# Kernel tuning notes

Measured on AMD Instinct MI355X. Metric: run time of the kernel, lower is better.

## Reference

```python
import jax, jax.numpy as jnp
import numpy as np

B, S, D, H = 4, 1024, 1024, 16
HD = D // H  # head_dim = 64
MASKED_BIAS = -10000.0


def setup_inputs() -> dict:
    key = jax.random.key(0)
    ks = jax.random.split(key, 7)
    sc = 0.02
    return {
        "hidden_states": jax.random.normal(ks[0], (B, S, D), jnp.float32),
        "textual_key": jax.random.normal(ks[1], (B, H, S, HD), jnp.float32),
        "textual_value": jax.random.normal(ks[2], (B, H, S, HD), jnp.float32),
        "Wc": jax.random.normal(ks[3], (D, 3 * D), jnp.float32) * sc,  # Conv1D c_attn
        "bc": jnp.zeros((3 * D,), jnp.float32),
        "Wp": jax.random.normal(ks[4], (D, D), jnp.float32) * sc,  # Conv1D c_proj
        "bp": jnp.zeros((D,), jnp.float32),
    }


def reference(hidden_states, textual_key, textual_value, Wc, bc, Wp, bp):
    b, s, d = hidden_states.shape
    # Conv1D: x @ W + b, then split into q, k, v
    qkv = hidden_states @ Wc + bc  # [B,S,3D]
    q, k, v = jnp.split(qkv, 3, axis=-1)

    def split_heads(t):  # [B,S,D] -> [B,H,S,HD]
        return t.reshape(b, s, H, HD).transpose(0, 2, 1, 3)

    q, k, v = split_heads(q), split_heads(k), split_heads(v)

    # cross-key scores against textual past + fused elementwise self-term
    text_w = jnp.einsum("bhqd,bhkd->bhqk", q, textual_key)  # [B,H,S,S_kv]
    self_w = jnp.sum(q * k, axis=-1, keepdims=True)  # [B,H,S,1]
    attn_w = jnp.concatenate([text_w, self_w], axis=-1) / (HD ** 0.5)

    # nonResidual causal mask: bias[kl-ql:kl, 1:kl+1] (strict lower-tri since
    # columns are shifted by 1) concatenated with an always-true self column
    i = jnp.arange(s)
    causal = i[None, :] < i[:, None]  # [S,S_kv]: allow k < q (strict)
    mask = jnp.concatenate([causal, jnp.ones((s, 1), bool)], axis=-1)[None, None]
    attn_w = jnp.where(mask, attn_w, jnp.asarray(MASKED_BIAS, attn_w.dtype))
    attn_w = jax.nn.softmax(attn_w, axis=-1)

    w_rest, w_self = attn_w[..., :-1], attn_w[..., -1:]
    out = jnp.einsum("bhqk,bhkd->bhqd", w_rest, textual_value) + w_self * v

    out = out.transpose(0, 2, 1, 3).reshape(b, s, d)  # merge heads
    return out @ Wp + bp
```

## Files before the change

kernel.cpp:

```cpp
#include <hip/hip_runtime.h>

typedef __bf16 bf16_t;
typedef __bf16 bf16x8 __attribute__((ext_vector_type(8)));
typedef __bf16 bf16x4 __attribute__((ext_vector_type(4)));
typedef _Float16 f16x4 __attribute__((ext_vector_type(4)));
typedef _Float16 f16x8 __attribute__((ext_vector_type(8)));
typedef float f32x4 __attribute__((ext_vector_type(4)));

__device__ __forceinline__ void gl_lds16(const void* g, void* l) {
  __builtin_amdgcn_global_load_lds(
      (const __attribute__((address_space(1))) unsigned int*)g,
      (__attribute__((address_space(3))) unsigned int*)l, 16, 0, 0);
}

__global__ __launch_bounds__(256) void prep_kernel(
    const float* __restrict__ hs, const float* __restrict__ tk, const float* __restrict__ tv,
    const float* __restrict__ Wc, const float* __restrict__ Wp,
    bf16_t* __restrict__ Ahs, bf16_t* __restrict__ Ktb, _Float16* __restrict__ Vtb,
    bf16_t* __restrict__ WcT, bf16_t* __restrict__ WpT) {
  const int blk = blockIdx.x;
  const int tid = threadIdx.x;
  if (blk < 4096) {
    const float4* src = (blk < 2048) ? (const float4*)hs : (const float4*)tk;
    bf16x8* dst = (blk < 2048) ? (bf16x8*)Ahs : (bf16x8*)Ktb;
    int i = (blk & 2047) * 256 + tid;
    float4 v0 = src[2 * i], v1 = src[2 * i + 1];
    bf16x8 o;
    o[0] = (bf16_t)v0.x; o[1] = (bf16_t)v0.y; o[2] = (bf16_t)v0.z; o[3] = (bf16_t)v0.w;
    o[4] = (bf16_t)v1.x; o[5] = (bf16_t)v1.y; o[6] = (bf16_t)v1.z; o[7] = (bf16_t)v1.w;
    dst[i] = o;
  } else {
    __shared__ float tile[32][65];
    const float* in; bf16_t* out; int C, r0, c0; size_t base = 0; bool isV = false;
    if (blk < 5632) {
      int t = blk - 4096; in = Wc; out = WcT; C = 3072;
      r0 = (t / 96) * 64; c0 = (t % 96) * 32;
    } else if (blk < 6144) {
      int t = blk - 5632; in = Wp; out = WpT; C = 1024;
      r0 = (t >> 5) * 64; c0 = (t & 31) * 32;
    } else {
      int t = blk - 6144; int z = t >> 5, rest = t & 31;
      in = tv; out = nullptr; isV = true; C = 64; base = (size_t)z * 65536;
      r0 = (rest >> 1) * 64; c0 = (rest & 1) * 32;
    }
    {
      int rr = tid >> 2, cq = (tid & 3) << 3;
      const float* sp = in + base + (size_t)(r0 + rr) * C + c0 + cq;
      float4 v0 = *(const float4*)sp, v1 = *(const float4*)(sp + 4);
      tile[cq + 0][rr] = v0.x; tile[cq + 1][rr] = v0.y;
      tile[cq + 2][rr] = v0.z; tile[cq + 3][rr] = v0.w;
      tile[cq + 4][rr] = v1.x; tile[cq + 5][rr] = v1.y;
      tile[cq + 6][rr] = v1.z; tile[cq + 7][rr] = v1.w;
    }
    __syncthreads();
    int y = tid >> 3, l = tid & 7;
    if (isV) {
      f16x8 o;
#pragma unroll
      for (int j = 0; j < 8; j++) {
        int k = ((l & 4) << 3) | ((j & 4) << 2) | ((l & 2) << 2) | ((l & 1) << 2) | (j & 3);
        o[j] = (_Float16)tile[y][k];
      }
      *(f16x8*)(Vtb + base + (size_t)(c0 + y) * 1024 + r0 + (l << 3)) = o;
    } else {
      const float* rowp = &tile[y][l << 3];
      bf16x8 o;
#pragma unroll
      for (int j = 0; j < 8; j++) o[j] = (bf16_t)rowp[j];
      *(bf16x8*)(out + (size_t)(c0 + y) * 1024 + r0 + (l << 3)) = o;
    }
  }
}

#define ATTN_M 12.0f
__global__ __launch_bounds__(512, 4) void fused_attn_kernel(
    const bf16_t* __restrict__ Ahs, const bf16_t* __restrict__ WcT,
    const float* __restrict__ bc,
    const bf16_t* __restrict__ Ktxt, const _Float16* __restrict__ VtxtT,
    bf16_t* __restrict__ Aout) {
  const int bh = blockIdx.x;
  const int y = blockIdx.y;
  const int qt = (y < 4) ? y : 11 - y;
  const int b = bh >> 4, h = bh & 15;
  const int tid = threadIdx.x, wave = tid >> 6, lane = tid & 63;
  const int c = lane & 15, qd = lane >> 4;
  const int i_base = qt * 128 + wave * 16;
  const int kt_max = 2 * qt + 1;
  const int m0 = b * 1024 + qt * 128;

  const bf16_t* Ktb = Ktxt + (size_t)bh * 65536;
  const _Float16* Vtb = VtxtT + (size_t)bh * 65536;

  __shared__ __align__(16) char pool[49152];
  bf16_t* Asm = (bf16_t*)pool;
  bf16_t* Bsm = (bf16_t*)(pool + 16384);
  bf16_t* Qsm = (bf16_t*)pool;
  bf16_t* KsmB = (bf16_t*)(pool + 16384);
  _Float16* VsmB = (_Float16*)(pool + 32768);

  f32x4 acc[12];
#pragma unroll
  for (int j = 0; j < 12; j++) acc[j] = (f32x4){0.f, 0.f, 0.f, 0.f};

  for (int kt = 0; kt < 16; kt++) {
#pragma unroll
    for (int p = 0; p < 2; p++) {
      int chunk = p * 512 + tid;
      int row = chunk >> 3, sb = chunk & 7, kb = sb ^ (row & 7);
      gl_lds16(Ahs + (size_t)(m0 + row) * 1024 + kt * 64 + kb * 8, Asm + chunk * 8);
    }
#pragma unroll
    for (int p = 0; p < 3; p++) {
      int chunk = p * 512 + tid;
      int brow = chunk >> 3, sb = chunk & 7, kb = sb ^ (brow & 7);
      int wrow = (brow >> 6) * 1024 + h * 64 + (brow & 63);
      gl_lds16(WcT + (size_t)wrow * 1024 + kt * 64 + kb * 8, Bsm + chunk * 8);
    }
    __syncthreads();
#pragma unroll
    for (int kk = 0; kk < 2; kk++) {
      int arow = wave * 16 + c;
      bf16x8 af = *(const bf16x8*)(&Asm[arow * 64 + (((4 * kk + qd) ^ (arow & 7)) << 3)]);
#pragma unroll
      for (int j = 0; j < 12; j++) {
        int brow = 16 * j + c;
        bf16x8 bf = *(const bf16x8*)(&Bsm[brow * 64 + (((4 * kk + qd) ^ (brow & 7)) << 3)]);
        acc[j] = __builtin_amdgcn_mfma_f32_16x16x32_bf16(af, bf, acc[j], 0, 0, 0);
      }
    }
    __syncthreads();
  }

  {
    int row = tid >> 3, sb = tid & 7, kb = sb ^ (row & 7);
    gl_lds16(Ktb + (size_t)row * 64 + kb * 8, KsmB + tid * 8);
    gl_lds16(Vtb + (size_t)row * 1024 + kb * 8, VsmB + tid * 8);
  }

#pragma unroll
  for (int j = 0; j < 12; j++) {
    float bv = bc[(j >> 2) * 1024 + h * 64 + 16 * (j & 3) + c];
#pragma unroll
    for (int r = 0; r < 4; r++) acc[j][r] += bv;
  }

  float wself[4];
#pragma unroll
  for (int r = 0; r < 4; r++) {
    float part = acc[0][r] * acc[4][r] + acc[1][r] * acc[5][r] +
                 acc[2][r] * acc[6][r] + acc[3][r] * acc[7][r];
#pragma unroll
    for (int mk = 1; mk < 16; mk <<= 1) part += __shfl_xor(part, mk, 64);
    wself[r] = __expf(part * 0.125f - ATTN_M);
  }

  f32x4 O[4];
#pragma unroll
  for (int u = 0; u < 4; u++)
#pragma unroll
    for (int r = 0; r < 4; r++) O[u][r] = wself[r] * acc[8 + u][r];

  bf16_t* Qw = Qsm + wave * 1024;
#pragma unroll
  for (int j = 0; j < 4; j++) {
#pragma unroll
    for (int r = 0; r < 4; r++) {
      int ql = 4 * qd + r, d = 16 * j + c;
      int ch = (d >> 3) ^ (ql & 7);
      Qw[ql * 64 + (ch << 3) + (d & 7)] = (bf16_t)acc[j][r];
    }
  }
  bf16x8 aq[2];
#pragma unroll
  for (int kk = 0; kk < 2; kk++) {
    int ch = (4 * kk + qd) ^ (c & 7);
    aq[kk] = *(const bf16x8*)(&Qw[c * 64 + (ch << 3)]);
  }

  float l_loc = 0.f;
  for (int kt = 0; kt <= kt_max; kt++) {
    __syncthreads();
    if (kt < kt_max) {
      int nb = (kt + 1) & 1;
      int row = tid >> 3, sb = tid & 7, kb = sb ^ (row & 7);
      gl_lds16(Ktb + (size_t)((kt + 1) * 64 + row) * 64 + kb * 8, KsmB + nb * 4096 + tid * 8);
      gl_lds16(Vtb + (size_t)row * 1024 + (kt + 1) * 64 + kb * 8, VsmB + nb * 4096 + tid * 8);
    }
    if (64 * kt >= i_base + 16) continue;
    const bf16_t* Ks = KsmB + (kt & 1) * 4096;
    const _Float16* Vs = VsmB + (kt & 1) * 4096;

    f32x4 sc[4];
#pragma unroll
    for (int t = 0; t < 4; t++) sc[t] = (f32x4){0.f, 0.f, 0.f, 0.f};
#pragma unroll
    for (int kk = 0; kk < 2; kk++) {
#pragma unroll
      for (int t = 0; t < 4; t++) {
        int row = 16 * t + c;
        bf16x8 bk = *(const bf16x8*)(&Ks[row * 64 + (((4 * kk + qd) ^ (row & 7)) << 3)]);
        sc[t] = __builtin_amdgcn_mfma_f32_16x16x32_bf16(bk, aq[kk], sc[t], 0, 0, 0);
      }
    }
    const bool edge = (64 * kt + 63 >= i_base);
    f16x4 pa[4];
    if (!edge) {
#pragma unroll
      for (int t = 0; t < 4; t++)
#pragma unroll
        for (int r = 0; r < 4; r++) {
          float p = __expf(sc[t][r] * 0.125f - ATTN_M);
          l_loc += p;
          pa[t][r] = (_Float16)p;
        }
    } else {
#pragma unroll
      for (int t = 0; t < 4; t++)
#pragma unroll
        for (int r = 0; r < 4; r++) {
          bool masked = (64 * kt + 16 * t + 4 * qd + r >= i_base + c);
          float p = masked ? 0.f : __expf(sc[t][r] * 0.125f - ATTN_M);
          l_loc += p;
          pa[t][r] = (_Float16)p;
        }
    }
#pragma unroll
    for (int tp = 0; tp < 2; tp++) {
#pragma unroll
      for (int u = 0; u < 4; u++) {
        int row = 16 * u + c;
        f16x8 vv = *(const f16x8*)(&Vs[row * 64 + (((4 * tp + qd) ^ (row & 7)) << 3)]);
        f16x4 vlo = __builtin_shufflevector(vv, vv, 0, 1, 2, 3);
        f16x4 vhi = __builtin_shufflevector(vv, vv, 4, 5, 6, 7);
        O[u] = __builtin_amdgcn_mfma_f32_16x16x16f16(pa[2 * tp], vlo, O[u], 0, 0, 0);
        O[u] = __builtin_amdgcn_mfma_f32_16x16x16f16(pa[2 * tp + 1], vhi, O[u], 0, 0, 0);
      }
    }
  }

  l_loc += __shfl_xor(l_loc, 16, 64);
  l_loc += __shfl_xor(l_loc, 32, 64);
#pragma unroll
  for (int r = 0; r < 4; r++) {
    float lq = __shfl(l_loc, 4 * qd + r, 16);
    float inv = 1.0f / (lq + wself[r]);
    int i = i_base + 4 * qd + r;
#pragma unroll
    for (int u = 0; u < 4; u++)
      Aout[((size_t)b * 1024 + i) * 1024 + h * 64 + 16 * u + c] = (bf16_t)(O[u][r] * inv);
  }
}

__global__ __launch_bounds__(256) void gemm_out_kernel(
    const bf16_t* __restrict__ A, const bf16_t* __restrict__ Bt, const float* __restrict__ bias,
    float* __restrict__ out) {
  __shared__ bf16_t Asm[2][4096];
  __shared__ bf16_t Bsm[2][8192];
  const int tid = threadIdx.x;
  const int wave = tid >> 6, lane = tid & 63;
  const int c = lane & 15, qd = lane >> 4;
  const int wn = wave * 32;
  const int m0 = blockIdx.y * 64, n0 = blockIdx.x * 128;

  f32x4 acc[4][2];
#pragma unroll
  for (int i = 0; i < 4; i++)
#pragma unroll
    for (int j = 0; j < 2; j++) acc[i][j] = (f32x4){0.f, 0.f, 0.f, 0.f};

#pragma unroll
  for (int p = 0; p < 2; p++) {
    int chunk = p * 256 + tid;
    int row = chunk >> 3, sb = chunk & 7, kb = sb ^ (row & 7);
    gl_lds16(A + (size_t)(m0 + row) * 1024 + kb * 8, &Asm[0][chunk * 8]);
  }
#pragma unroll
  for (int p = 0; p < 4; p++) {
    int chunk = p * 256 + tid;
    int row = chunk >> 3, sb = chunk & 7, kb = sb ^ (row & 7);
    gl_lds16(Bt + (size_t)(n0 + row) * 1024 + kb * 8, &Bsm[0][chunk * 8]);
  }
  for (int it = 0; it < 16; it++) {
    __syncthreads();
    if (it < 15) {
      int nbuf = (it + 1) & 1, kt = (it + 1) * 64;
#pragma unroll
      for (int p = 0; p < 2; p++) {
        int chunk = p * 256 + tid;
        int row = chunk >> 3, sb = chunk & 7, kb = sb ^ (row & 7);
        gl_lds16(A + (size_t)(m0 + row) * 1024 + kt + kb * 8, &Asm[nbuf][chunk * 8]);
      }
#pragma unroll
      for (int p = 0; p < 4; p++) {
        int chunk = p * 256 + tid;
        int row = chunk >> 3, sb = chunk & 7, kb = sb ^ (row & 7);
        gl_lds16(Bt + (size_t)(n0 + row) * 1024 + kt + kb * 8, &Bsm[nbuf][chunk * 8]);
      }
    }
    const int bs = it & 1;
#pragma unroll
    for (int kk = 0; kk < 2; kk++) {
      bf16x8 af[4], bfr[2];
#pragma unroll
      for (int i = 0; i < 4; i++) {
        int row = 16 * i + c;
        af[i] = *(const bf16x8*)(&Asm[bs][row * 64 + (((4 * kk + qd) ^ (row & 7)) << 3)]);
      }
#pragma unroll
      for (int j = 0; j < 2; j++) {
        int row = wn + 16 * j + c;
        bfr[j] = *(const bf16x8*)(&Bsm[bs][row * 64 + (((4 * kk + qd) ^ (row & 7)) << 3)]);
      }
#pragma unroll
      for (int i = 0; i < 4; i++)
#pragma unroll
        for (int j = 0; j < 2; j++)
          acc[i][j] = __builtin_amdgcn_mfma_f32_16x16x32_bf16(af[i], bfr[j], acc[i][j], 0, 0, 0);
    }
  }
#pragma unroll
  for (int j = 0; j < 2; j++) {
    int n = n0 + wn + 16 * j + c;
    float bv = bias[n];
#pragma unroll
    for (int i = 0; i < 4; i++) {
#pragma unroll
      for (int r = 0; r < 4; r++) {
        int m = m0 + 16 * i + 4 * qd + r;
        out[(size_t)m * 1024 + n] = acc[i][j][r] + bv;
      }
    }
  }
}

extern "C" void kernel_launch(void* const* d_in, const int* in_sizes, int n_in,
                              void* d_out, int out_size, void* d_ws, size_t ws_size,
                              hipStream_t stream) {
  const float* hs = (const float*)d_in[0];
  const float* tk = (const float*)d_in[1];
  const float* tv = (const float*)d_in[2];
  const float* Wc = (const float*)d_in[3];
  const float* bc = (const float*)d_in[4];
  const float* Wp = (const float*)d_in[5];
  const float* bp = (const float*)d_in[6];
  float* out = (float*)d_out;

  bf16_t* ws = (bf16_t*)d_ws;
  const size_t M1 = 1u << 20;
  bf16_t* Ahs  = ws;
  bf16_t* WcT  = ws + 4 * M1;
  bf16_t* WpT  = ws + 7 * M1;
  bf16_t* Ktb  = ws + 8 * M1;
  _Float16* Vtb = (_Float16*)(ws + 12 * M1);
  bf16_t* Aout = ws + 28 * M1;

  prep_kernel<<<8192, 256, 0, stream>>>(hs, tk, tv, Wc, Wp, Ahs, Ktb, Vtb, WcT, WpT);
  fused_attn_kernel<<<dim3(64, 8), 512, 0, stream>>>(Ahs, WcT, bc, Ktb, Vtb, Aout);
  gemm_out_kernel<<<dim3(8, 64), 256, 0, stream>>>(Aout, WpT, bp, out);
}
```

Baseline: 174.7 us.

## Use 2D warp tiling for fused QKV GEMM with 4 waves, 32 queries each

The fused attention kernel drops from 8 waves to 4 waves per block. Each wave now computes a 64x96 sub-tile of the 128x192 QKV projection in a 2D warp layout, instead of a 16x192 strip, so each loaded A/B fragment is reused by more MFMAs and LDS traffic per MFMA falls. The QKV tile is staged through a swizzled LDS buffer so each wave can gather Q, the self-key and V for its 32 query rows. In the attention loop each K/V fragment load now feeds two query groups. The costs are higher register pressure (24 accumulators), an extra LDS round-trip with syncs, and half as many waves per block for latency hiding.

Result: no change. 174.8 us (+0.1%).

```diff
diff --git a/kernel.cpp b/kernel.cpp
--- a/kernel.cpp
+++ b/kernel.cpp
@@ -2,7 +2,6 @@
 
 typedef __bf16 bf16_t;
 typedef __bf16 bf16x8 __attribute__((ext_vector_type(8)));
-typedef __bf16 bf16x4 __attribute__((ext_vector_type(4)));
 typedef _Float16 f16x4 __attribute__((ext_vector_type(4)));
 typedef _Float16 f16x8 __attribute__((ext_vector_type(8)));
 typedef float f32x4 __attribute__((ext_vector_type(4)));
@@ -73,7 +72,7 @@
 }
 
 #define ATTN_M 12.0f
-__global__ __launch_bounds__(512, 4) void fused_attn_kernel(
+__global__ __launch_bounds__(256, 2) void fused_attn_kernel(
     const bf16_t* __restrict__ Ahs, const bf16_t* __restrict__ WcT,
     const float* __restrict__ bc,
     const bf16_t* __restrict__ Ktxt, const _Float16* __restrict__ VtxtT,
@@ -84,9 +83,9 @@
   const int b = bh >> 4, h = bh & 15;
   const int tid = threadIdx.x, wave = tid >> 6, lane = tid & 63;
   const int c = lane & 15, qd = lane >> 4;
-  const int i_base = qt * 128 + wave * 16;
+  const int m0 = b * 1024 + qt * 128;
+  const int i_base2 = qt * 128 + 32 * wave;
   const int kt_max = 2 * qt + 1;
-  const int m0 = b * 1024 + qt * 128;
 
   const bf16_t* Ktb = Ktxt + (size_t)bh * 65536;
   const _Float16* Vtb = VtxtT + (size_t)bh * 65536;
@@ -94,24 +93,27 @@
   __shared__ __align__(16) char pool[49152];
   bf16_t* Asm = (bf16_t*)pool;
   bf16_t* Bsm = (bf16_t*)(pool + 16384);
-  bf16_t* Qsm = (bf16_t*)pool;
-  bf16_t* KsmB = (bf16_t*)(pool + 16384);
-  _Float16* VsmB = (_Float16*)(pool + 32768);
-
-  f32x4 acc[12];
-#pragma unroll
-  for (int j = 0; j < 12; j++) acc[j] = (f32x4){0.f, 0.f, 0.f, 0.f};
+  bf16_t* T = (bf16_t*)pool;
+  bf16_t* KsmB = (bf16_t*)pool;
+  _Float16* VsmB = (_Float16*)(pool + 16384);
+
+  const int wm = (wave & 1) * 64, wn = (wave >> 1) * 96;
+  f32x4 acc[4][6];
+#pragma unroll
+  for (int i = 0; i < 4; i++)
+#pragma unroll
+    for (int j = 0; j < 6; j++) acc[i][j] = (f32x4){0.f, 0.f, 0.f, 0.f};
 
   for (int kt = 0; kt < 16; kt++) {
 #pragma unroll
-    for (int p = 0; p < 2; p++) {
-      int chunk = p * 512 + tid;
+    for (int p = 0; p < 4; p++) {
+      int chunk = p * 256 + tid;
       int row = chunk >> 3, sb = chunk & 7, kb = sb ^ (row & 7);
       gl_lds16(Ahs + (size_t)(m0 + row) * 1024 + kt * 64 + kb * 8, Asm + chunk * 8);
     }
 #pragma unroll
-    for (int p = 0; p < 3; p++) {
-      int chunk = p * 512 + tid;
+    for (int p = 0; p < 6; p++) {
+      int chunk = p * 256 + tid;
       int brow = chunk >> 3, sb = chunk & 7, kb = sb ^ (brow & 7);
       int wrow = (brow >> 6) * 1024 + h * 64 + (brow & 63);
       gl_lds16(WcT + (size_t)wrow * 1024 + kt * 64 + kb * 8, Bsm + chunk * 8);
@@ -119,110 +121,148 @@
     __syncthreads();
 #pragma unroll
     for (int kk = 0; kk < 2; kk++) {
-      int arow = wave * 16 + c;
-      bf16x8 af = *(const bf16x8*)(&Asm[arow * 64 + (((4 * kk + qd) ^ (arow & 7)) << 3)]);
-#pragma unroll
-      for (int j = 0; j < 12; j++) {
-        int brow = 16 * j + c;
-        bf16x8 bf = *(const bf16x8*)(&Bsm[brow * 64 + (((4 * kk + qd) ^ (brow & 7)) << 3)]);
-        acc[j] = __builtin_amdgcn_mfma_f32_16x16x32_bf16(af, bf, acc[j], 0, 0, 0);
-      }
+      bf16x8 af[4], bfr[6];
+#pragma unroll
+      for (int i = 0; i < 4; i++) {
+        int row = wm + 16 * i + c;
+        af[i] = *(const bf16x8*)(&Asm[row * 64 + (((4 * kk + qd) ^ (row & 7)) << 3)]);
+      }
+#pragma unroll
+      for (int j = 0; j < 6; j++) {
+        int row = wn + 16 * j + c;
+        bfr[j] = *(const bf16x8*)(&Bsm[row * 64 + (((4 * kk + qd) ^ (row & 7)) << 3)]);
+      }
+#pragma unroll
+      for (int i = 0; i < 4; i++)
+#pragma unroll
+        for (int j = 0; j < 6; j++)
+          acc[i][j] = __builtin_amdgcn_mfma_f32_16x16x32_bf16(af[i], bfr[j], acc[i][j], 0, 0, 0);
     }
     __syncthreads();
   }
 
-  {
-    int row = tid >> 3, sb = tid & 7, kb = sb ^ (row & 7);
-    gl_lds16(Ktb + (size_t)row * 64 + kb * 8, KsmB + tid * 8);
-    gl_lds16(Vtb + (size_t)row * 1024 + kb * 8, VsmB + tid * 8);
-  }
-
-#pragma unroll
-  for (int j = 0; j < 12; j++) {
-    float bv = bc[(j >> 2) * 1024 + h * 64 + 16 * (j & 3) + c];
-#pragma unroll
-    for (int r = 0; r < 4; r++) acc[j][r] += bv;
-  }
-
-  float wself[4];
-#pragma unroll
-  for (int r = 0; r < 4; r++) {
-    float part = acc[0][r] * acc[4][r] + acc[1][r] * acc[5][r] +
-                 acc[2][r] * acc[6][r] + acc[3][r] * acc[7][r];
-#pragma unroll
-    for (int mk = 1; mk < 16; mk <<= 1) part += __shfl_xor(part, mk, 64);
-    wself[r] = __expf(part * 0.125f - ATTN_M);
-  }
-
-  f32x4 O[4];
-#pragma unroll
-  for (int u = 0; u < 4; u++)
-#pragma unroll
-    for (int r = 0; r < 4; r++) O[u][r] = wself[r] * acc[8 + u][r];
-
-  bf16_t* Qw = Qsm + wave * 1024;
-#pragma unroll
-  for (int j = 0; j < 4; j++) {
-#pragma unroll
-    for (int r = 0; r < 4; r++) {
-      int ql = 4 * qd + r, d = 16 * j + c;
-      int ch = (d >> 3) ^ (ql & 7);
-      Qw[ql * 64 + (ch << 3) + (d & 7)] = (bf16_t)acc[j][r];
-    }
-  }
-  bf16x8 aq[2];
-#pragma unroll
-  for (int kk = 0; kk < 2; kk++) {
-    int ch = (4 * kk + qd) ^ (c & 7);
-    aq[kk] = *(const bf16x8*)(&Qw[c * 64 + (ch << 3)]);
-  }
-
-  float l_loc = 0.f;
+#pragma unroll
+  for (int j = 0; j < 6; j++) {
+    int col = wn + 16 * j + c;
+    float bv = bc[(col >> 6) * 1024 + h * 64 + (col & 63)];
+    int chq = (col >> 3) & 24;
+    int chl = (col >> 3) & 7;
+#pragma unroll
+    for (int i = 0; i < 4; i++) {
+#pragma unroll
+      for (int r = 0; r < 4; r++) {
+        int row = wm + 16 * i + 4 * qd + r;
+        int ch = chq | (chl ^ (row & 7));
+        T[row * 192 + ch * 8 + (col & 7)] = (bf16_t)(acc[i][j][r] + bv);
+      }
+    }
+  }
+  __syncthreads();
+
+  bf16x8 aq[2][2];
+  float wsc[2];
+  float ws[2][4];
+#pragma unroll
+  for (int g = 0; g < 2; g++) {
+    int row = 32 * wave + 16 * g + c;
+    float part = 0.f;
+#pragma unroll
+    for (int kk = 0; kk < 2; kk++) {
+      int ch = (4 * kk + qd) ^ (row & 7);
+      aq[g][kk] = *(const bf16x8*)(&T[row * 192 + ch * 8]);
+      bf16x8 kf = *(const bf16x8*)(&T[row * 192 + (8 | ch) * 8]);
+#pragma unroll
+      for (int jj = 0; jj < 8; jj++) part += (float)aq[g][kk][jj] * (float)kf[jj];
+    }
+    part += __shfl_xor(part, 16, 64);
+    part += __shfl_xor(part, 32, 64);
+    wsc[g] = __expf(part * 0.125f - ATTN_M);
+#pragma unroll
+    for (int r = 0; r < 4; r++) ws[g][r] = __shfl(wsc[g], 4 * qd + r, 16);
+  }
+  f32x4 O[2][4];
+#pragma unroll
+  for (int g = 0; g < 2; g++) {
+#pragma unroll
+    for (int u = 0; u < 4; u++) {
+#pragma unroll
+      for (int r = 0; r < 4; r++) {
+        int row = 32 * wave + 16 * g + 4 * qd + r;
+        int ch = 16 | ((2 * u + (c >> 3)) ^ (row & 7));
+        O[g][u][r] = ws[g][r] * (float)T[row * 192 + ch * 8 + (c & 7)];
+      }
+    }
+  }
+  __syncthreads();
+
+#pragma unroll
+  for (int p = 0; p < 2; p++) {
+    int chunk = p * 256 + tid;
+    int row = chunk >> 3, sb = chunk & 7, kb = sb ^ (row & 7);
+    gl_lds16(Ktb + (size_t)row * 64 + kb * 8, KsmB + chunk * 8);
+    gl_lds16(Vtb + (size_t)row * 1024 + kb * 8, VsmB + chunk * 8);
+  }
+
+  float l_loc[2] = {0.f, 0.f};
   for (int kt = 0; kt <= kt_max; kt++) {
     __syncthreads();
     if (kt < kt_max) {
       int nb = (kt + 1) & 1;
-      int row = tid >> 3, sb = tid & 7, kb = sb ^ (row & 7);
-      gl_lds16(Ktb + (size_t)((kt + 1) * 64 + row) * 64 + kb * 8, KsmB + nb * 4096 + tid * 8);
-      gl_lds16(Vtb + (size_t)row * 1024 + (kt + 1) * 64 + kb * 8, VsmB + nb * 4096 + tid * 8);
-    }
-    if (64 * kt >= i_base + 16) continue;
+#pragma unroll
+      for (int p = 0; p < 2; p++) {
+        int chunk = p * 256 + tid;
+        int row = chunk >> 3, sb = chunk & 7, kb = sb ^ (row & 7);
+        gl_lds16(Ktb + (size_t)((kt + 1) * 64 + row) * 64 + kb * 8,
+                 KsmB + nb * 4096 + chunk * 8);
+        gl_lds16(Vtb + (size_t)row * 1024 + (kt + 1) * 64 + kb * 8,
+                 VsmB + nb * 4096 + chunk * 8);
+      }
+    }
+    if (64 * kt >= i_base2 + 32) continue;
     const bf16_t* Ks = KsmB + (kt & 1) * 4096;
     const _Float16* Vs = VsmB + (kt & 1) * 4096;
 
-    f32x4 sc[4];
-#pragma unroll
-    for (int t = 0; t < 4; t++) sc[t] = (f32x4){0.f, 0.f, 0.f, 0.f};
+    f32x4 sc[2][4];
+#pragma unroll
+    for (int t = 0; t < 4; t++) {
+      sc[0][t] = (f32x4){0.f, 0.f, 0.f, 0.f};
+      sc[1][t] = (f32x4){0.f, 0.f, 0.f, 0.f};
+    }
 #pragma unroll
     for (int kk = 0; kk < 2; kk++) {
 #pragma unroll
       for (int t = 0; t < 4; t++) {
         int row = 16 * t + c;
         bf16x8 bk = *(const bf16x8*)(&Ks[row * 64 + (((4 * kk + qd) ^ (row & 7)) << 3)]);
-        sc[t] = __builtin_amdgcn_mfma_f32_16x16x32_bf16(bk, aq[kk], sc[t], 0, 0, 0);
-      }
-    }
-    const bool edge = (64 * kt + 63 >= i_base);
-    f16x4 pa[4];
+        sc[0][t] = __builtin_amdgcn_mfma_f32_16x16x32_bf16(bk, aq[0][kk], sc[0][t], 0, 0, 0);
+        sc[1][t] = __builtin_amdgcn_mfma_f32_16x16x32_bf16(bk, aq[1][kk], sc[1][t], 0, 0, 0);
+      }
+    }
+    const bool edge = (64 * kt + 63 >= i_base2);
+    f16x4 pa[2][4];
     if (!edge) {
 #pragma unroll
-      for (int t = 0; t < 4; t++)
-#pragma unroll
-        for (int r = 0; r < 4; r++) {
-          float p = __expf(sc[t][r] * 0.125f - ATTN_M);
-          l_loc += p;
-          pa[t][r] = (_Float16)p;
-        }
+      for (int g = 0; g < 2; g++)
+#pragma unroll
+        for (int t = 0; t < 4; t++)
+#pragma unroll
+          for (int r = 0; r < 4; r++) {
+            float p = __expf(sc[g][t][r] * 0.125f - ATTN_M);
+            l_loc[g] += p;
+            pa[g][t][r] = (_Float16)p;
+          }
     } else {
 #pragma unroll
-      for (int t = 0; t < 4; t++)
-#pragma unroll
-        for (int r = 0; r < 4; r++) {
-          bool masked = (64 * kt + 16 * t + 4 * qd + r >= i_base + c);
-          float p = masked ? 0.f : __expf(sc[t][r] * 0.125f - ATTN_M);
-          l_loc += p;
-          pa[t][r] = (_Float16)p;
-        }
+      for (int g = 0; g < 2; g++)
+#pragma unroll
+        for (int t = 0; t < 4; t++)
+#pragma unroll
+          for (int r = 0; r < 4; r++) {
+            bool masked = (64 * kt + 16 * t + 4 * qd + r >= i_base2 + 16 * g + c);
+            float p = masked ? 0.f : __expf(sc[g][t][r] * 0.125f - ATTN_M);
+            l_loc[g] += p;
+            pa[g][t][r] = (_Float16)p;
+          }
     }
 #pragma unroll
     for (int tp = 0; tp < 2; tp++) {
@@ -232,22 +272,28 @@
         f16x8 vv = *(const f16x8*)(&Vs[row * 64 + (((4 * tp + qd) ^ (row & 7)) << 3)]);
         f16x4 vlo = __builtin_shufflevector(vv, vv, 0, 1, 2, 3);
         f16x4 vhi = __builtin_shufflevector(vv, vv, 4, 5, 6, 7);
-        O[u] = __builtin_amdgcn_mfma_f32_16x16x16f16(pa[2 * tp], vlo, O[u], 0, 0, 0);
-        O[u] = __builtin_amdgcn_mfma_f32_16x16x16f16(pa[2 * tp + 1], vhi, O[u], 0, 0, 0);
-      }
-    }
-  }
-
-  l_loc += __shfl_xor(l_loc, 16, 64);
-  l_loc += __shfl_xor(l_loc, 32, 64);
-#pragma unroll
-  for (int r = 0; r < 4; r++) {
-    float lq = __shfl(l_loc, 4 * qd + r, 16);
-    float inv = 1.0f / (lq + wself[r]);
-    int i = i_base + 4 * qd + r;
-#pragma unroll
-    for (int u = 0; u < 4; u++)
-      Aout[((size_t)b * 1024 + i) * 1024 + h * 64 + 16 * u + c] = (bf16_t)(O[u][r] * inv);
+        O[0][u] = __builtin_amdgcn_mfma_f32_16x16x16f16(pa[0][2 * tp], vlo, O[0][u], 0, 0, 0);
+        O[0][u] = __builtin_amdgcn_mfma_f32_16x16x16f16(pa[0][2 * tp + 1], vhi, O[0][u], 0, 0, 0);
+        O[1][u] = __builtin_amdgcn_mfma_f32_16x16x16f16(pa[1][2 * tp], vlo, O[1][u], 0, 0, 0);
+        O[1][u] = __builtin_amdgcn_mfma_f32_16x16x16f16(pa[1][2 * tp + 1], vhi, O[1][u], 0, 0, 0);
+      }
+    }
+  }
+
+#pragma unroll
+  for (int g = 0; g < 2; g++) {
+    float l = l_loc[g];
+    l += __shfl_xor(l, 16, 64);
+    l += __shfl_xor(l, 32, 64);
+#pragma unroll
+    for (int r = 0; r < 4; r++) {
+      float lq = __shfl(l, 4 * qd + r, 16);
+      float inv = 1.0f / (lq + ws[g][r]);
+      int i = i_base2 + 16 * g + 4 * qd + r;
+#pragma unroll
+      for (int u = 0; u < 4; u++)
+        Aout[((size_t)b * 1024 + i) * 1024 + h * 64 + 16 * u + c] = (bf16_t)(O[g][u][r] * inv);
+    }
   }
 }
 
@@ -355,6 +401,6 @@
   bf16_t* Aout = ws + 28 * M1;
 
   prep_kernel<<<8192, 256, 0, stream>>>(hs, tk, tv, Wc, Wp, Ahs, Ktb, Vtb, WcT, WpT);
-  fused_attn_kernel<<<dim3(64, 8), 512, 0, stream>>>(Ahs, WcT, bc, Ktb, Vtb, Aout);
+  fused_attn_kernel<<<dim3(64, 8), 256, 0, stream>>>(Ahs, WcT, bc, Ktb, Vtb, Aout);
   gemm_out_kernel<<<dim3(8, 64), 256, 0, stream>>>(Aout, WpT, bp, out);
 }
```
